# Performance work log

Measured on AMD Instinct MI355X. Metric: run time of the kernel, lower is better.

## Reference

```python
import jax, jax.numpy as jnp
import numpy as np

D_MODEL = 1024
N_HEADS = 16
D_HEAD = 64
B, S = 8, 1024
EPS = 1.1920929e-07  # torch.finfo(float32).eps, RMSNorm default eps=None


def setup_inputs() -> dict:
    key = jax.random.key(0)
    k1, k2, k3 = jax.random.split(key, 3)
    x = jax.random.normal(k1, (B, S, D_MODEL), dtype=jnp.float32)
    W_qkv = jax.random.normal(k2, (3 * N_HEADS * D_HEAD, D_MODEL), dtype=jnp.float32) * 0.02
    b_qkv = jnp.zeros((3 * N_HEADS * D_HEAD,), dtype=jnp.float32)
    W_o = jax.random.normal(k3, (D_MODEL, N_HEADS * D_HEAD), dtype=jnp.float32) * 0.02
    b_o = jnp.zeros((D_MODEL,), dtype=jnp.float32)
    return {"x": x, "W_qkv": W_qkv, "b_qkv": b_qkv, "W_o": W_o, "b_o": b_o}


def reference(x, W_qkv, b_qkv, W_o, b_o):
    # RMSNorm, no affine
    normed = x * jax.lax.rsqrt(jnp.mean(x * x, axis=-1, keepdims=True) + EPS)
    qkv = normed @ W_qkv.T + b_qkv                       # [b, s, 3*H*Dh]
    # packing order '(n_heads d_head n_qkv)' -> reshape (H, Dh, 3), unbind last
    qkv = qkv.reshape(*qkv.shape[:-1], N_HEADS, D_HEAD, 3)
    q, k, v = qkv[..., 0], qkv[..., 1], qkv[..., 2]       # [b, s, H, Dh]
    scores = jnp.einsum('bqhd,bkhd->bhqk', q, k)          # no 1/sqrt(d) scaling
    seq = x.shape[-2]
    causal_mask = jnp.triu(jnp.ones((seq, seq), dtype=bool), k=1)  # True above diag
    scores = jnp.where(causal_mask, -jnp.inf, scores)
    # NOTE: softmax over the QUERY axis (dim=-2), faithful to the source
    attn = jax.nn.softmax(scores, axis=-2)                # [b, h, q, k]
    z = jnp.einsum('bhqk,bkhd->bqhd', attn, v)            # [b, q, H, Dh]
    z = z.reshape(*z.shape[:-2], N_HEADS * D_HEAD)
    return z @ W_o.T + b_o
```

## Files before the change

### kernel.cpp

```cpp
#include <hip/hip_runtime.h>
#include <hip/hip_bf16.h>

typedef _Float16 f16;
typedef _Float16 f16x8 __attribute__((ext_vector_type(8)));
typedef _Float16 f16x4 __attribute__((ext_vector_type(4)));
typedef float f32x4 __attribute__((ext_vector_type(4)));

constexpr int Bb = 8, Ss = 1024, Hh = 16, DH = 64, DM = 1024, N3 = 3072;
constexpr int Mm = Bb * Ss;
constexpr float EPS = 1.1920929e-07f;

__device__ __forceinline__ void gll16(const f16* g, f16* l) {
    __builtin_amdgcn_global_load_lds(
        (__attribute__((address_space(1))) void*)(g),
        (__attribute__((address_space(3))) void*)(l), 16, 0, 0);
}

__global__ void rmscast_kernel(const float* __restrict__ x, f16* __restrict__ xh) {
    const int row = blockIdx.x;
    const int t = threadIdx.x;
    float4 v = *(const float4*)(x + (size_t)row * DM + t * 4);
    float s = v.x * v.x + v.y * v.y + v.z * v.z + v.w * v.w;
#pragma unroll
    for (int o = 32; o > 0; o >>= 1) s += __shfl_down(s, o, 64);
    __shared__ float red[4];
    if ((t & 63) == 0) red[t >> 6] = s;
    __syncthreads();
    float tot = red[0] + red[1] + red[2] + red[3];
    float sc = rsqrtf(tot * (1.0f / DM) + EPS);
    f16x4 hv = {(f16)(v.x * sc), (f16)(v.y * sc), (f16)(v.z * sc), (f16)(v.w * sc)};
    *(f16x4*)(xh + (size_t)row * DM + t * 4) = hv;
}

__global__ void castw_kernel(const float* __restrict__ Wqkv, const float* __restrict__ Wo,
                             f16* __restrict__ wq, f16* __restrict__ wo) {
    int i = blockIdx.x * 256 + threadIdx.x;
    const int n1 = (N3 * DM) / 4;
    if (i < n1) {
        float4 v = ((const float4*)Wqkv)[i];
        f16x4 h = {(f16)v.x, (f16)v.y, (f16)v.z, (f16)v.w};
        ((f16x4*)wq)[i] = h;
    } else {
        int j = i - n1;
        float4 v = ((const float4*)Wo)[j];
        f16x4 h = {(f16)v.x, (f16)v.y, (f16)v.z, (f16)v.w};
        ((f16x4*)wo)[j] = h;
    }
}

__launch_bounds__(256, 2)
__global__ void qkv_gemm(const f16* __restrict__ xh, const f16* __restrict__ wq,
                         const float* __restrict__ bqkv, f16* __restrict__ qk,
                         f16* __restrict__ vT) {
    __shared__ __align__(16) f16 As[128 * 64];
    __shared__ __align__(16) f16 Bs[128 * 64];
    const int t = threadIdx.x, lane = t & 63, w = t >> 6;
    const int gm0 = blockIdx.y * 128, gn0 = blockIdx.x * 128;
    const int wm = (w >> 1) * 64, wn = (w & 1) * 64;
    const int srow = lane >> 3, sslot = (lane & 7) ^ srow;
    const int r15 = lane & 15, cs = lane >> 4;

    const f16* Ag = xh + (size_t)(gm0 + srow) * DM + sslot * 8;
    const f16* Bg = wq + (size_t)(gn0 + srow) * DM + sslot * 8;

    int aoff[4][2], boff[4][2];
#pragma unroll
    for (int i = 0; i < 4; ++i) {
        int Ra = wm + i * 16 + r15;
        aoff[i][0] = Ra * 64 + ((cs ^ (Ra & 7)) * 8);
        aoff[i][1] = Ra * 64 + (((cs + 4) ^ (Ra & 7)) * 8);
        int Rb = wn + i * 16 + r15;
        boff[i][0] = Rb * 64 + ((cs ^ (Rb & 7)) * 8);
        boff[i][1] = Rb * 64 + (((cs + 4) ^ (Rb & 7)) * 8);
    }
    f32x4 acc[4][4] = {};

    for (int k0 = 0; k0 < DM; k0 += 64) {
        __syncthreads();
#pragma unroll
        for (int j = 0; j < 4; ++j) {
            int c = w * 4 + j;
            gll16(Ag + (size_t)c * 8 * DM + k0, As + c * 512);
            gll16(Bg + (size_t)c * 8 * DM + k0, Bs + c * 512);
        }
        __syncthreads();
#pragma unroll
        for (int half = 0; half < 2; ++half) {
            f16x8 af[4], bf[4];
#pragma unroll
            for (int i = 0; i < 4; ++i) af[i] = *(const f16x8*)&As[aoff[i][half]];
#pragma unroll
            for (int i = 0; i < 4; ++i) bf[i] = *(const f16x8*)&Bs[boff[i][half]];
#pragma unroll
            for (int mi = 0; mi < 4; ++mi)
#pragma unroll
                for (int ni = 0; ni < 4; ++ni)
                    acc[mi][ni] = __builtin_amdgcn_mfma_f32_16x16x32_f16(af[mi], bf[ni], acc[mi][ni], 0, 0, 0);
        }
    }
#pragma unroll
    for (int mi = 0; mi < 4; ++mi) {
#pragma unroll
        for (int ni = 0; ni < 4; ++ni) {
            int jcol = gn0 + wn + ni * 16 + r15;
            float bb = bqkv[jcol];
            int h = jcol / 192, r = jcol % 192;
            int d = r / 3, which = r % 3;
            int m0 = gm0 + wm + mi * 16 + cs * 4;
            int b = m0 >> 10, s0 = m0 & 1023;
            int bh = b * Hh + h;
            if (which == 2) {
                f16x4 pv = {(f16)(acc[mi][ni][0] + bb), (f16)(acc[mi][ni][1] + bb),
                            (f16)(acc[mi][ni][2] + bb), (f16)(acc[mi][ni][3] + bb)};
                *(f16x4*)(vT + ((size_t)bh * DH + d) * Ss + s0) = pv;
            } else {
                size_t base = ((size_t)which * (Bb * Hh) + bh) * (size_t)(Ss * DH) + (size_t)s0 * DH + d;
#pragma unroll
                for (int jj = 0; jj < 4; ++jj)
                    qk[base + (size_t)jj * DH] = (f16)(acc[mi][ni][jj] + bb);
            }
        }
    }
}

__launch_bounds__(512, 2)
__global__ void colstats_kernel(const f16* __restrict__ qk, float* __restrict__ cbuf) {
    __shared__ __align__(16) f16 KsA[128 * 64];
    __shared__ __align__(16) f16 KsB[128 * 64];
    __shared__ __align__(16) f16 Qs[2][64 * 64];
    const int t = threadIdx.x, lane = t & 63, w = t >> 6;
    const int r15 = lane & 15, cs = lane >> 4;
    const int srow = lane >> 3, sslot = (lane & 7) ^ srow;
    const int bh = blockIdx.y, si = blockIdx.x;
    const int kA0 = si * 128, kB0 = (7 - si) * 128;
    const size_t hs = (size_t)(Bb * Hh) * (Ss * DH);
    const f16* qb = qk + (size_t)bh * (Ss * DH);
    const f16* kb = qb + hs;
    const int qt0 = 2 * si;

    gll16(kb + (size_t)(kA0 + w * 16 + srow) * DH + sslot * 8, KsA + (2 * w) * 512);
    gll16(kb + (size_t)(kA0 + w * 16 + 8 + srow) * DH + sslot * 8, KsA + (2 * w + 1) * 512);
    gll16(kb + (size_t)(kB0 + w * 16 + srow) * DH + sslot * 8, KsB + (2 * w) * 512);
    gll16(kb + (size_t)(kB0 + w * 16 + 8 + srow) * DH + sslot * 8, KsB + (2 * w + 1) * 512);
    gll16(qb + (size_t)(qt0 * 64 + w * 8 + srow) * DH + sslot * 8, Qs[0] + w * 512);
    __syncthreads();
    const int Rk = w * 16 + r15;
    f16x8 kfA0 = *(const f16x8*)&KsA[Rk * 64 + ((cs ^ (Rk & 7)) * 8)];
    f16x8 kfA1 = *(const f16x8*)&KsA[Rk * 64 + (((cs + 4) ^ (Rk & 7)) * 8)];
    f16x8 kfB0 = *(const f16x8*)&KsB[Rk * 64 + ((cs ^ (Rk & 7)) * 8)];
    f16x8 kfB1 = *(const f16x8*)&KsB[Rk * 64 + (((cs + 4) ^ (Rk & 7)) * 8)];
    const int kwA = kA0 + w * 16, kglobA = kwA + r15;
    const int kwB = kB0 + w * 16, kglobB = kwB + r15;
    float la = 0.0f, lb = 0.0f;
    int cur = 0;

    for (int qt = qt0; qt < 16; ++qt) {
        if (qt + 1 < 16)
            gll16(qb + (size_t)((qt + 1) * 64 + w * 8 + srow) * DH + sslot * 8,
                  Qs[cur ^ 1] + w * 512);
        const bool engA = (qt * 64 + 63 >= kwA);
        const bool engB = (qt * 64 + 63 >= kwB);
        if (engA || engB) {
#pragma unroll
            for (int qs = 0; qs < 4; ++qs) {
                const int qb16 = qt * 64 + qs * 16;
                const bool nA = engA && (qb16 + 15 >= kwA);
                const bool nB = engB && (qb16 + 15 >= kwB);
                if (!(nA || nB)) continue;
                int Ra = qs * 16 + r15;
                f16x8 a0 = *(const f16x8*)&Qs[cur][Ra * 64 + ((cs ^ (Ra & 7)) * 8)];
                f16x8 a1 = *(const f16x8*)&Qs[cur][Ra * 64 + (((cs + 4) ^ (Ra & 7)) * 8)];
                if (nA) {
                    f32x4 sf = {};
                    sf = __builtin_amdgcn_mfma_f32_16x16x32_f16(a0, kfA0, sf, 0, 0, 0);
                    sf = __builtin_amdgcn_mfma_f32_16x16x32_f16(a1, kfA1, sf, 0, 0, 0);
#pragma unroll
                    for (int j = 0; j < 4; ++j) {
                        int q = qb16 + cs * 4 + j;
                        la += (q >= kglobA) ? __expf(sf[j]) : 0.0f;
                    }
                }
                if (nB) {
                    f32x4 sf = {};
                    sf = __builtin_amdgcn_mfma_f32_16x16x32_f16(a0, kfB0, sf, 0, 0, 0);
                    sf = __builtin_amdgcn_mfma_f32_16x16x32_f16(a1, kfB1, sf, 0, 0, 0);
#pragma unroll
                    for (int j = 0; j < 4; ++j) {
                        int q = qb16 + cs * 4 + j;
                        lb += (q >= kglobB) ? __expf(sf[j]) : 0.0f;
                    }
                }
            }
        }
        __syncthreads();
        cur ^= 1;
    }
    la += __shfl_xor(la, 16, 64);
    la += __shfl_xor(la, 32, 64);
    lb += __shfl_xor(lb, 16, 64);
    lb += __shfl_xor(lb, 32, 64);
    if (cs == 0) {
        cbuf[bh * Ss + kglobA] = logf(la);
        cbuf[bh * Ss + kglobB] = logf(lb);
    }
}

__launch_bounds__(512, 2)
__global__ void attnz_kernel(const f16* __restrict__ qk, const f16* __restrict__ vT,
                             const float* __restrict__ cbuf, f16* __restrict__ z) {
    __shared__ __align__(16) f16 QsA[128 * 64];
    __shared__ __align__(16) f16 QsB[128 * 64];
    __shared__ __align__(16) f16 Ks[64 * 64];
    __shared__ __align__(16) f16 Vs[64 * 64];
    __shared__ __align__(16) float cb[1024];
    const int t = threadIdx.x, lane = t & 63, w = t >> 6;
    const int r15 = lane & 15, cs = lane >> 4;
    const int srow = lane >> 3, sslot = (lane & 7) ^ srow;
    const int bh = blockIdx.y, si = blockIdx.x;
    const int qtA = si, qtB = 7 - si;
    const size_t hs = (size_t)(Bb * Hh) * (Ss * DH);
    const f16* qb = qk + (size_t)bh * (Ss * DH);
    const f16* kb = qb + hs;
    const f16* vb = vT + (size_t)bh * (DH * Ss);

    gll16(qb + (size_t)(qtA * 128 + w * 16 + srow) * DH + sslot * 8, QsA + (2 * w) * 512);
    gll16(qb + (size_t)(qtA * 128 + w * 16 + 8 + srow) * DH + sslot * 8, QsA + (2 * w + 1) * 512);
    gll16(qb + (size_t)(qtB * 128 + w * 16 + srow) * DH + sslot * 8, QsB + (2 * w) * 512);
    gll16(qb + (size_t)(qtB * 128 + w * 16 + 8 + srow) * DH + sslot * 8, QsB + (2 * w + 1) * 512);
    gll16(kb + (size_t)(w * 8 + srow) * DH + sslot * 8, Ks + w * 512);
    gll16(vb + (size_t)(w * 8 + srow) * Ss + sslot * 8, Vs + w * 512);
    {
        float2 c2 = *(const float2*)(cbuf + bh * Ss + t * 2);
        *(float2*)&cb[t * 2] = c2;
    }
    __syncthreads();
    const int Rq = w * 16 + r15;
    f16x8 aqA0 = *(const f16x8*)&QsA[Rq * 64 + ((cs ^ (Rq & 7)) * 8)];
    f16x8 aqA1 = *(const f16x8*)&QsA[Rq * 64 + (((cs + 4) ^ (Rq & 7)) * 8)];
    f16x8 aqB0 = *(const f16x8*)&QsB[Rq * 64 + ((cs ^ (Rq & 7)) * 8)];
    f16x8 aqB1 = *(const f16x8*)&QsB[Rq * 64 + (((cs + 4) ^ (Rq & 7)) * 8)];
    f32x4 accA[4] = {}, accB[4] = {};
    const int qwA = qtA * 128 + w * 16, qA = qwA + r15;
    const int qwB = qtB * 128 + w * 16, qB = qwB + r15;
    const int nktA = 2 * qtA + 2, nktB = 2 * qtB + 2;
    const int sAl = ((cs & 1) * 2) * 16 + r15;
    const int sBl = sAl + 16;
    const bool hi = (cs >> 1) != 0;

    for (int kt = 0; kt < nktB; ++kt) {
        if (kt) {
            __syncthreads();
            gll16(kb + (size_t)(kt * 64 + w * 8 + srow) * DH + sslot * 8, Ks + w * 512);
            gll16(vb + (size_t)(w * 8 + srow) * Ss + kt * 64 + sslot * 8, Vs + w * 512);
            __syncthreads();
        }
        const int kb0 = kt * 64;
        const bool doA = (kt < nktA) && (kb0 <= qwA + 15);
        const bool doB = (kb0 <= qwB + 15);
        if (!(doA || doB)) continue;

        unsigned pkA[4][2], pkB[4][2];
#pragma unroll
        for (int tl = 0; tl < 4; ++tl) {
            const int kbase = kb0 + tl * 16;
            const bool nA = doA && (kbase <= qwA + 15);
            const bool nB = doB && (kbase <= qwB + 15);
            pkA[tl][0] = 0u; pkA[tl][1] = 0u;
            pkB[tl][0] = 0u; pkB[tl][1] = 0u;
            if (!(nA || nB)) continue;
            int Rk2 = tl * 16 + r15;
            f16x8 kf0 = *(const f16x8*)&Ks[Rk2 * 64 + ((cs ^ (Rk2 & 7)) * 8)];
            f16x8 kf1 = *(const f16x8*)&Ks[Rk2 * 64 + (((cs + 4) ^ (Rk2 & 7)) * 8)];
            f32x4 cv = *(const f32x4*)&cb[kbase + cs * 4];
            if (nA) {
                f32x4 sf = {};
                sf = __builtin_amdgcn_mfma_f32_16x16x32_f16(kf0, aqA0, sf, 0, 0, 0);
                sf = __builtin_amdgcn_mfma_f32_16x16x32_f16(kf1, aqA1, sf, 0, 0, 0);
                f16 p[4];
#pragma unroll
                for (int j = 0; j < 4; ++j) {
                    int k = kbase + cs * 4 + j;
                    p[j] = (f16)((k <= qA) ? __expf(sf[j] - cv[j]) : 0.0f);
                }
                union { f16 h[2]; unsigned u; } u0, u1;
                u0.h[0] = p[0]; u0.h[1] = p[1];
                u1.h[0] = p[2]; u1.h[1] = p[3];
                pkA[tl][0] = u0.u; pkA[tl][1] = u1.u;
            }
            if (nB) {
                f32x4 sf = {};
                sf = __builtin_amdgcn_mfma_f32_16x16x32_f16(kf0, aqB0, sf, 0, 0, 0);
                sf = __builtin_amdgcn_mfma_f32_16x16x32_f16(kf1, aqB1, sf, 0, 0, 0);
                f16 p[4];
#pragma unroll
                for (int j = 0; j < 4; ++j) {
                    int k = kbase + cs * 4 + j;
                    p[j] = (f16)((k <= qB) ? __expf(sf[j] - cv[j]) : 0.0f);
                }
                union { f16 h[2]; unsigned u; } u0, u1;
                u0.h[0] = p[0]; u0.h[1] = p[1];
                u1.h[0] = p[2]; u1.h[1] = p[3];
                pkB[tl][0] = u0.u; pkB[tl][1] = u1.u;
            }
        }
        f16x8 bfA[2], bfB[2];
        bool uA[2], uB[2];
#pragma unroll
        for (int c = 0; c < 2; ++c) {
            uA[c] = doA && (kb0 + c * 32 <= qwA + 15);
            uB[c] = doB && (kb0 + c * 32 <= qwB + 15);
            if (uA[c]) {
                unsigned a0 = (unsigned)__shfl((int)pkA[2 * c][0], sAl, 64);
                unsigned a1 = (unsigned)__shfl((int)pkA[2 * c][1], sAl, 64);
                unsigned a2 = (unsigned)__shfl((int)pkA[2 * c][0], sBl, 64);
                unsigned a3 = (unsigned)__shfl((int)pkA[2 * c][1], sBl, 64);
                unsigned b0_ = (unsigned)__shfl((int)pkA[2 * c + 1][0], sAl, 64);
                unsigned b1_ = (unsigned)__shfl((int)pkA[2 * c + 1][1], sAl, 64);
                unsigned b2_ = (unsigned)__shfl((int)pkA[2 * c + 1][0], sBl, 64);
                unsigned b3_ = (unsigned)__shfl((int)pkA[2 * c + 1][1], sBl, 64);
                union { unsigned u[4]; f16x8 v; } bf;
                bf.u[0] = hi ? b0_ : a0;
                bf.u[1] = hi ? b1_ : a1;
                bf.u[2] = hi ? b2_ : a2;
                bf.u[3] = hi ? b3_ : a3;
                bfA[c] = bf.v;
            }
            if (uB[c]) {
                unsigned a0 = (unsigned)__shfl((int)pkB[2 * c][0], sAl, 64);
                unsigned a1 = (unsigned)__shfl((int)pkB[2 * c][1], sAl, 64);
                unsigned a2 = (unsigned)__shfl((int)pkB[2 * c][0], sBl, 64);
                unsigned a3 = (unsigned)__shfl((int)pkB[2 * c][1], sBl, 64);
                unsigned b0_ = (unsigned)__shfl((int)pkB[2 * c + 1][0], sAl, 64);
                unsigned b1_ = (unsigned)__shfl((int)pkB[2 * c + 1][1], sAl, 64);
                unsigned b2_ = (unsigned)__shfl((int)pkB[2 * c + 1][0], sBl, 64);
                unsigned b3_ = (unsigned)__shfl((int)pkB[2 * c + 1][1], sBl, 64);
                union { unsigned u[4]; f16x8 v; } bf;
                bf.u[0] = hi ? b0_ : a0;
                bf.u[1] = hi ? b1_ : a1;
                bf.u[2] = hi ? b2_ : a2;
                bf.u[3] = hi ? b3_ : a3;
                bfB[c] = bf.v;
            }
        }
#pragma unroll
        for (int dt = 0; dt < 4; ++dt) {
            int Rv = dt * 16 + r15;
            f16x8 v0 = *(const f16x8*)&Vs[Rv * 64 + ((cs ^ (Rv & 7)) * 8)];
            f16x8 v1 = *(const f16x8*)&Vs[Rv * 64 + (((4 + cs) ^ (Rv & 7)) * 8)];
            if (uA[0]) accA[dt] = __builtin_amdgcn_mfma_f32_16x16x32_f16(v0, bfA[0], accA[dt], 0, 0, 0);
            if (uA[1]) accA[dt] = __builtin_amdgcn_mfma_f32_16x16x32_f16(v1, bfA[1], accA[dt], 0, 0, 0);
            if (uB[0]) accB[dt] = __builtin_amdgcn_mfma_f32_16x16x32_f16(v0, bfB[0], accB[dt], 0, 0, 0);
            if (uB[1]) accB[dt] = __builtin_amdgcn_mfma_f32_16x16x32_f16(v1, bfB[1], accB[dt], 0, 0, 0);
        }
    }
    const int b = bh >> 4, h = bh & 15;
#pragma unroll
    for (int dt = 0; dt < 4; ++dt) {
        f16x4 zvA = {(f16)accA[dt][0], (f16)accA[dt][1], (f16)accA[dt][2], (f16)accA[dt][3]};
        *(f16x4*)(z + ((size_t)(b * Ss + qA)) * DM + h * DH + dt * 16 + cs * 4) = zvA;
        f16x4 zvB = {(f16)accB[dt][0], (f16)accB[dt][1], (f16)accB[dt][2], (f16)accB[dt][3]};
        *(f16x4*)(z + ((size_t)(b * Ss + qB)) * DM + h * DH + dt * 16 + cs * 4) = zvB;
    }
}

__launch_bounds__(256, 2)
__global__ void out_gemm(const f16* __restrict__ z, const f16* __restrict__ wo,
                         const float* __restrict__ bo, float* __restrict__ out) {
    __shared__ __align__(16) f16 As[128 * 64];
    __shared__ __align__(16) f16 Bs[128 * 64];
    const int t = threadIdx.x, lane = t & 63, w = t >> 6;
    const int gm0 = blockIdx.y * 128, gn0 = blockIdx.x * 128;
    const int wm = (w >> 1) * 64, wn = (w & 1) * 64;
    const int srow = lane >> 3, sslot = (lane & 7) ^ srow;
    const int r15 = lane & 15, cs = lane >> 4;

    const f16* Ag = z + (size_t)(gm0 + srow) * DM + sslot * 8;
    const f16* Bg = wo + (size_t)(gn0 + srow) * DM + sslot * 8;

    int aoff[4][2], boff[4][2];
#pragma unroll
    for (int i = 0; i < 4; ++i) {
        int Ra = wm + i * 16 + r15;
        aoff[i][0] = Ra * 64 + ((cs ^ (Ra & 7)) * 8);
        aoff[i][1] = Ra * 64 + (((cs + 4) ^ (Ra & 7)) * 8);
        int Rb = wn + i * 16 + r15;
        boff[i][0] = Rb * 64 + ((cs ^ (Rb & 7)) * 8);
        boff[i][1] = Rb * 64 + (((cs + 4) ^ (Rb & 7)) * 8);
    }
    f32x4 acc[4][4] = {};

    for (int k0 = 0; k0 < DM; k0 += 64) {
        __syncthreads();
#pragma unroll
        for (int j = 0; j < 4; ++j) {
            int c = w * 4 + j;
            gll16(Ag + (size_t)c * 8 * DM + k0, As + c * 512);
            gll16(Bg + (size_t)c * 8 * DM + k0, Bs + c * 512);
        }
        __syncthreads();
#pragma unroll
        for (int half = 0; half < 2; ++half) {
            f16x8 af[4], bf[4];
#pragma unroll
            for (int i = 0; i < 4; ++i) af[i] = *(const f16x8*)&As[aoff[i][half]];
#pragma unroll
            for (int i = 0; i < 4; ++i) bf[i] = *(const f16x8*)&Bs[boff[i][half]];
#pragma unroll
            for (int mi = 0; mi < 4; ++mi)
#pragma unroll
                for (int ni = 0; ni < 4; ++ni)
                    acc[mi][ni] = __builtin_amdgcn_mfma_f32_16x16x32_f16(af[mi], bf[ni], acc[mi][ni], 0, 0, 0);
        }
    }
#pragma unroll
    for (int mi = 0; mi < 4; ++mi) {
#pragma unroll
        for (int ni = 0; ni < 4; ++ni) {
            int n = gn0 + wn + ni * 16 + r15;
            float bb = bo[n];
#pragma unroll
            for (int jj = 0; jj < 4; ++jj) {
                int m = gm0 + wm + mi * 16 + cs * 4 + jj;
                out[(size_t)m * DM + n] = acc[mi][ni][jj] + bb;
            }
        }
    }
}

extern "C" void kernel_launch(void* const* d_in, const int* in_sizes, int n_in,
                              void* d_out, int out_size, void* d_ws, size_t ws_size,
                              hipStream_t stream) {
    (void)in_sizes; (void)n_in; (void)out_size; (void)ws_size;
    const float* x    = (const float*)d_in[0];
    const float* Wqkv = (const float*)d_in[1];
    const float* bqkv = (const float*)d_in[2];
    const float* Wo   = (const float*)d_in[3];
    const float* bo   = (const float*)d_in[4];
    float* out = (float*)d_out;

    char* ws = (char*)d_ws;
    f16* xh   = (f16*)ws;
    f16* z    = (f16*)ws;
    f16* wq   = (f16*)(ws + 16777216);
    f16* wo   = (f16*)(ws + 23068672);
    f16* qk   = (f16*)(ws + 25165824);
    f16* vT   = (f16*)(ws + 58720256);
    float* cbuf = (float*)(ws + 75497472);

    rmscast_kernel<<<Mm, 256, 0, stream>>>(x, xh);
    castw_kernel<<<(N3 * DM + DM * DM) / 1024, 256, 0, stream>>>(Wqkv, Wo, wq, wo);
    qkv_gemm<<<dim3(N3 / 128, Mm / 128), 256, 0, stream>>>(xh, wq, bqkv, qk, vT);
    colstats_kernel<<<dim3(4, Bb * Hh), 512, 0, stream>>>(qk, cbuf);
    attnz_kernel<<<dim3(4, Bb * Hh), 512, 0, stream>>>(qk, vT, cbuf, z);
    out_gemm<<<dim3(DM / 128, Mm / 128), 256, 0, stream>>>(z, wo, bo, out);
}
```

Baseline: 202.1 us.

## Replace both GEMMs with a double-buffered 256x256 tiled kernel template

Replaces the QKV and output GEMMs with one templated kernel. It uses 256x256 block tiles, 8 waves, and a double-buffered LDS pipeline that issues the global-to-LDS loads for the next K tile while computing the current one. It also adds manual waitcnt/barrier scheduling and MFMA priority hints. The larger tiles raise data reuse per block and the prefetch hides load latency. The cost is fewer blocks (only 128 for the output GEMM on 256 CUs) and higher register and LDS use per block.

```diff
diff --git a/kernel.cpp b/kernel.cpp
--- a/kernel.cpp
+++ b/kernel.cpp
@@ -48,76 +48,121 @@
     }
 }
 
-__launch_bounds__(256, 2)
-__global__ void qkv_gemm(const f16* __restrict__ xh, const f16* __restrict__ wq,
-                         const float* __restrict__ bqkv, f16* __restrict__ qk,
-                         f16* __restrict__ vT) {
-    __shared__ __align__(16) f16 As[128 * 64];
-    __shared__ __align__(16) f16 Bs[128 * 64];
+template <int EPI>
+__launch_bounds__(512, 1)
+__global__ void gemm8p(const f16* __restrict__ Aglob, const f16* __restrict__ Bglob,
+                       const float* __restrict__ bias, void* __restrict__ out0,
+                       f16* __restrict__ vT) {
+    __shared__ __align__(16) f16 As[2][256 * 64];
+    __shared__ __align__(16) f16 Bs[2][256 * 64];
     const int t = threadIdx.x, lane = t & 63, w = t >> 6;
-    const int gm0 = blockIdx.y * 128, gn0 = blockIdx.x * 128;
-    const int wm = (w >> 1) * 64, wn = (w & 1) * 64;
+    const int gm0 = blockIdx.y * 256, gn0 = blockIdx.x * 256;
+    const int wm = (w >> 2) * 128, wn = (w & 3) * 64;
     const int srow = lane >> 3, sslot = (lane & 7) ^ srow;
     const int r15 = lane & 15, cs = lane >> 4;
 
-    const f16* Ag = xh + (size_t)(gm0 + srow) * DM + sslot * 8;
-    const f16* Bg = wq + (size_t)(gn0 + srow) * DM + sslot * 8;
-
-    int aoff[4][2], boff[4][2];
-#pragma unroll
-    for (int i = 0; i < 4; ++i) {
-        int Ra = wm + i * 16 + r15;
-        aoff[i][0] = Ra * 64 + ((cs ^ (Ra & 7)) * 8);
-        aoff[i][1] = Ra * 64 + (((cs + 4) ^ (Ra & 7)) * 8);
-        int Rb = wn + i * 16 + r15;
-        boff[i][0] = Rb * 64 + ((cs ^ (Rb & 7)) * 8);
-        boff[i][1] = Rb * 64 + (((cs + 4) ^ (Rb & 7)) * 8);
-    }
-    f32x4 acc[4][4] = {};
-
-    for (int k0 = 0; k0 < DM; k0 += 64) {
-        __syncthreads();
-#pragma unroll
-        for (int j = 0; j < 4; ++j) {
-            int c = w * 4 + j;
-            gll16(Ag + (size_t)c * 8 * DM + k0, As + c * 512);
-            gll16(Bg + (size_t)c * 8 * DM + k0, Bs + c * 512);
-        }
-        __syncthreads();
-#pragma unroll
-        for (int half = 0; half < 2; ++half) {
-            f16x8 af[4], bf[4];
-#pragma unroll
-            for (int i = 0; i < 4; ++i) af[i] = *(const f16x8*)&As[aoff[i][half]];
-#pragma unroll
-            for (int i = 0; i < 4; ++i) bf[i] = *(const f16x8*)&Bs[boff[i][half]];
+    const f16* Ag = Aglob + (size_t)(gm0 + srow) * DM + sslot * 8;
+    const f16* Bg = Bglob + (size_t)(gn0 + srow) * DM + sslot * 8;
+
+    f32x4 acc[8][4] = {};
+
+#pragma unroll
+    for (int j = 0; j < 4; ++j) {
+        int c = w * 4 + j;
+        gll16(Ag + (size_t)c * 8 * DM, &As[0][c * 512]);
+        gll16(Bg + (size_t)c * 8 * DM, &Bs[0][c * 512]);
+    }
+
+    for (int kt = 0; kt < 16; ++kt) {
+        const int cur = kt & 1;
+        if (kt + 1 < 16) {
+            const int nb = cur ^ 1, k0n = (kt + 1) * 64;
+#pragma unroll
+            for (int j = 0; j < 4; ++j) {
+                int c = w * 4 + j;
+                gll16(Ag + (size_t)c * 8 * DM + k0n, &As[nb][c * 512]);
+                gll16(Bg + (size_t)c * 8 * DM + k0n, &Bs[nb][c * 512]);
+            }
+            asm volatile("s_waitcnt vmcnt(8)" ::: "memory");
+        } else {
+            asm volatile("s_waitcnt vmcnt(0)" ::: "memory");
+        }
+        __builtin_amdgcn_s_barrier();
+        __builtin_amdgcn_sched_barrier(0);
+
+        f16x8 bf[4][2];
+#pragma unroll
+        for (int i = 0; i < 4; ++i) {
+            int Rb = wn + i * 16 + r15;
+            bf[i][0] = *(const f16x8*)&Bs[cur][Rb * 64 + ((cs ^ (Rb & 7)) * 8)];
+            bf[i][1] = *(const f16x8*)&Bs[cur][Rb * 64 + (((cs + 4) ^ (Rb & 7)) * 8)];
+        }
+#pragma unroll
+        for (int mh = 0; mh < 2; ++mh) {
+            f16x8 af[4][2];
+#pragma unroll
+            for (int i = 0; i < 4; ++i) {
+                int Ra = wm + mh * 64 + i * 16 + r15;
+                af[i][0] = *(const f16x8*)&As[cur][Ra * 64 + ((cs ^ (Ra & 7)) * 8)];
+                af[i][1] = *(const f16x8*)&As[cur][Ra * 64 + (((cs + 4) ^ (Ra & 7)) * 8)];
+            }
+            __builtin_amdgcn_s_setprio(1);
 #pragma unroll
             for (int mi = 0; mi < 4; ++mi)
 #pragma unroll
-                for (int ni = 0; ni < 4; ++ni)
-                    acc[mi][ni] = __builtin_amdgcn_mfma_f32_16x16x32_f16(af[mi], bf[ni], acc[mi][ni], 0, 0, 0);
-        }
-    }
-#pragma unroll
-    for (int mi = 0; mi < 4; ++mi) {
-#pragma unroll
-        for (int ni = 0; ni < 4; ++ni) {
-            int jcol = gn0 + wn + ni * 16 + r15;
-            float bb = bqkv[jcol];
-            int h = jcol / 192, r = jcol % 192;
-            int d = r / 3, which = r % 3;
-            int m0 = gm0 + wm + mi * 16 + cs * 4;
-            int b = m0 >> 10, s0 = m0 & 1023;
-            int bh = b * Hh + h;
-            if (which == 2) {
-                f16x4 pv = {(f16)(acc[mi][ni][0] + bb), (f16)(acc[mi][ni][1] + bb),
-                            (f16)(acc[mi][ni][2] + bb), (f16)(acc[mi][ni][3] + bb)};
-                *(f16x4*)(vT + ((size_t)bh * DH + d) * Ss + s0) = pv;
-            } else {
-                size_t base = ((size_t)which * (Bb * Hh) + bh) * (size_t)(Ss * DH) + (size_t)s0 * DH + d;
-#pragma unroll
-                for (int jj = 0; jj < 4; ++jj)
-                    qk[base + (size_t)jj * DH] = (f16)(acc[mi][ni][jj] + bb);
+                for (int ni = 0; ni < 4; ++ni) {
+                    acc[mh * 4 + mi][ni] = __builtin_amdgcn_mfma_f32_16x16x32_f16(
+                        af[mi][0], bf[ni][0], acc[mh * 4 + mi][ni], 0, 0, 0);
+                    acc[mh * 4 + mi][ni] = __builtin_amdgcn_mfma_f32_16x16x32_f16(
+                        af[mi][1], bf[ni][1], acc[mh * 4 + mi][ni], 0, 0, 0);
+                }
+            __builtin_amdgcn_s_setprio(0);
+        }
+        asm volatile("s_waitcnt lgkmcnt(0)" ::: "memory");
+        __builtin_amdgcn_sched_barrier(0);
+        __builtin_amdgcn_s_barrier();
+        __builtin_amdgcn_sched_barrier(0);
+    }
+
+    if (EPI == 1) {
+        f16* qk = (f16*)out0;
+#pragma unroll
+        for (int mi = 0; mi < 8; ++mi) {
+#pragma unroll
+            for (int ni = 0; ni < 4; ++ni) {
+                int jcol = gn0 + wn + ni * 16 + r15;
+                float bb = bias[jcol];
+                int h = jcol / 192, r = jcol % 192;
+                int d = r / 3, which = r % 3;
+                int m0 = gm0 + wm + mi * 16 + cs * 4;
+                int b = m0 >> 10, s0 = m0 & 1023;
+                int bh = b * Hh + h;
+                if (which == 2) {
+                    f16x4 pv = {(f16)(acc[mi][ni][0] + bb), (f16)(acc[mi][ni][1] + bb),
+                                (f16)(acc[mi][ni][2] + bb), (f16)(acc[mi][ni][3] + bb)};
+                    *(f16x4*)(vT + ((size_t)bh * DH + d) * Ss + s0) = pv;
+                } else {
+                    size_t base = ((size_t)which * (Bb * Hh) + bh) * (size_t)(Ss * DH) +
+                                  (size_t)s0 * DH + d;
+#pragma unroll
+                    for (int jj = 0; jj < 4; ++jj)
+                        qk[base + (size_t)jj * DH] = (f16)(acc[mi][ni][jj] + bb);
+                }
+            }
+        }
+    } else {
+        float* out = (float*)out0;
+#pragma unroll
+        for (int mi = 0; mi < 8; ++mi) {
+#pragma unroll
+            for (int ni = 0; ni < 4; ++ni) {
+                int n = gn0 + wn + ni * 16 + r15;
+                float bb = bias[n];
+#pragma unroll
+                for (int jj = 0; jj < 4; ++jj) {
+                    int m = gm0 + wm + mi * 16 + cs * 4 + jj;
+                    out[(size_t)m * DM + n] = acc[mi][ni][jj] + bb;
+                }
             }
         }
     }
@@ -363,70 +408,6 @@
     }
 }
 
-__launch_bounds__(256, 2)
-__global__ void out_gemm(const f16* __restrict__ z, const f16* __restrict__ wo,
-                         const float* __restrict__ bo, float* __restrict__ out) {
-    __shared__ __align__(16) f16 As[128 * 64];
-    __shared__ __align__(16) f16 Bs[128 * 64];
-    const int t = threadIdx.x, lane = t & 63, w = t >> 6;
-    const int gm0 = blockIdx.y * 128, gn0 = blockIdx.x * 128;
-    const int wm = (w >> 1) * 64, wn = (w & 1) * 64;
-    const int srow = lane >> 3, sslot = (lane & 7) ^ srow;
-    const int r15 = lane & 15, cs = lane >> 4;
-
-    const f16* Ag = z + (size_t)(gm0 + srow) * DM + sslot * 8;
-    const f16* Bg = wo + (size_t)(gn0 + srow) * DM + sslot * 8;
-
-    int aoff[4][2], boff[4][2];
-#pragma unroll
-    for (int i = 0; i < 4; ++i) {
-        int Ra = wm + i * 16 + r15;
-        aoff[i][0] = Ra * 64 + ((cs ^ (Ra & 7)) * 8);
-        aoff[i][1] = Ra * 64 + (((cs + 4) ^ (Ra & 7)) * 8);
-        int Rb = wn + i * 16 + r15;
-        boff[i][0] = Rb * 64 + ((cs ^ (Rb & 7)) * 8);
-        boff[i][1] = Rb * 64 + (((cs + 4) ^ (Rb & 7)) * 8);
-    }
-    f32x4 acc[4][4] = {};
-
-    for (int k0 = 0; k0 < DM; k0 += 64) {
-        __syncthreads();
-#pragma unroll
-        for (int j = 0; j < 4; ++j) {
-            int c = w * 4 + j;
-            gll16(Ag + (size_t)c * 8 * DM + k0, As + c * 512);
-            gll16(Bg + (size_t)c * 8 * DM + k0, Bs + c * 512);
-        }
-        __syncthreads();
-#pragma unroll
-        for (int half = 0; half < 2; ++half) {
-            f16x8 af[4], bf[4];
-#pragma unroll
-            for (int i = 0; i < 4; ++i) af[i] = *(const f16x8*)&As[aoff[i][half]];
-#pragma unroll
-            for (int i = 0; i < 4; ++i) bf[i] = *(const f16x8*)&Bs[boff[i][half]];
-#pragma unroll
-            for (int mi = 0; mi < 4; ++mi)
-#pragma unroll
-                for (int ni = 0; ni < 4; ++ni)
-                    acc[mi][ni] = __builtin_amdgcn_mfma_f32_16x16x32_f16(af[mi], bf[ni], acc[mi][ni], 0, 0, 0);
-        }
-    }
-#pragma unroll
-    for (int mi = 0; mi < 4; ++mi) {
-#pragma unroll
-        for (int ni = 0; ni < 4; ++ni) {
-            int n = gn0 + wn + ni * 16 + r15;
-            float bb = bo[n];
-#pragma unroll
-            for (int jj = 0; jj < 4; ++jj) {
-                int m = gm0 + wm + mi * 16 + cs * 4 + jj;
-                out[(size_t)m * DM + n] = acc[mi][ni][jj] + bb;
-            }
-        }
-    }
-}
-
 extern "C" void kernel_launch(void* const* d_in, const int* in_sizes, int n_in,
                               void* d_out, int out_size, void* d_ws, size_t ws_size,
                               hipStream_t stream) {
@@ -449,8 +430,8 @@
 
     rmscast_kernel<<<Mm, 256, 0, stream>>>(x, xh);
     castw_kernel<<<(N3 * DM + DM * DM) / 1024, 256, 0, stream>>>(Wqkv, Wo, wq, wo);
-    qkv_gemm<<<dim3(N3 / 128, Mm / 128), 256, 0, stream>>>(xh, wq, bqkv, qk, vT);
+    gemm8p<1><<<dim3(N3 / 256, Mm / 256), 512, 0, stream>>>(xh, wq, bqkv, qk, vT);
     colstats_kernel<<<dim3(4, Bb * Hh), 512, 0, stream>>>(qk, cbuf);
     attnz_kernel<<<dim3(4, Bb * Hh), 512, 0, stream>>>(qk, vT, cbuf, z);
-    out_gemm<<<dim3(DM / 128, Mm / 128), 256, 0, stream>>>(z, wo, bo, out);
-}
+    gemm8p<0><<<dim3(DM / 256, Mm / 256), 512, 0, stream>>>(z, wo, bo, out, nullptr);
+}
```

Result: slower. 221.3 us (+9.5%).
